# Performance work log

Hardware: AMD Instinct MI355X
Metric: run time of the kernel (lower is better)

The kernel has to match this reference:

```python
import jax, jax.numpy as jnp
import numpy as np

HEAD_SIZE = 64
D_MODEL = 768


def setup_inputs() -> dict:
    key = jax.random.key(0)
    ks = jax.random.split(key, 7)
    x = jax.random.normal(ks[0], (8, 4096, D_MODEL), dtype=jnp.float32)
    def lin_init(kw, kb, fan_in, fan_out):
        bound = 1.0 / np.sqrt(fan_in)
        W = jax.random.uniform(kw, (fan_in, fan_out), minval=-bound, maxval=bound, dtype=jnp.float32)
        b = jax.random.uniform(kb, (fan_out,), minval=-bound, maxval=bound, dtype=jnp.float32)
        return W, b
    Wq, bq = lin_init(ks[1], ks[2], D_MODEL, HEAD_SIZE)
    Wk, bk = lin_init(ks[3], ks[4], D_MODEL, HEAD_SIZE)
    Wv, bv = lin_init(ks[5], ks[6], D_MODEL, HEAD_SIZE)
    return {"x": x, "Wq": Wq, "bq": bq, "Wk": Wk, "bk": bk, "Wv": Wv, "bv": bv}


def reference(x, Wq, bq, Wk, bk, Wv, bv):
    # x: [B, N, 768]; projections to [B, N, head_size]
    q = jnp.einsum("bnd,dh->bnh", x, Wq) + bq
    k = jnp.einsum("bnd,dh->bnh", x, Wk) + bk
    v = jnp.einsum("bnd,dh->bnh", x, Wv) + bv
    scale = 1.0 / jnp.sqrt(jnp.asarray(q.shape[-1], dtype=q.dtype))
    wei = jnp.einsum("bqh,bkh->bqk", q, k) * scale  # [B, N, N]
    wei = jax.nn.softmax(wei, axis=-1)
    out = jnp.einsum("bqk,bkh->bqh", wei, v)  # [B, N, head_size]
    return out
```

## Files before the change

### kernel.cpp

```cpp
#include <hip/hip_runtime.h>
#include <stdint.h>
#include <stddef.h>

typedef __bf16 bf16x8 __attribute__((ext_vector_type(8)));
typedef __bf16 bf16x4 __attribute__((ext_vector_type(4)));
typedef float  f32x4  __attribute__((ext_vector_type(4)));

#define MFMA16(A, B, C) __builtin_amdgcn_mfma_f32_16x16x32_bf16((A), (B), (C), 0, 0, 0)

#define QSCALE 0.18033688011112042f

#if __has_builtin(__builtin_amdgcn_exp2f)
__device__ __forceinline__ float fast_exp2(float x) {
    return __builtin_amdgcn_exp2f(x);
}
#else
__device__ __forceinline__ float fast_exp2(float x) {
    float r;
    asm("v_exp_f32 %0, %1" : "=v"(r) : "v"(x));
    return r;
}
#endif

__device__ __forceinline__ void async_copy16(__bf16* lds, const __bf16* g) {
    __builtin_amdgcn_global_load_lds(
        (const __attribute__((address_space(1))) void*)g,
        (__attribute__((address_space(3))) void*)lds,
        16, 0, 0);
}

__global__ __launch_bounds__(256) void qkv_proj_kernel(
    const float* __restrict__ x,
    const float* __restrict__ Wq, const float* __restrict__ bq,
    const float* __restrict__ Wk, const float* __restrict__ bk,
    const float* __restrict__ Wv, const float* __restrict__ bv,
    __bf16* __restrict__ Qg, __bf16* __restrict__ Kg, __bf16* __restrict__ Vcg)
{
    __shared__ __bf16 xs[64][40];
    __shared__ __bf16 wt[192][40];

    const int tid  = threadIdx.x;
    const int wid  = tid >> 6;
    const int lane = tid & 63;
    const int l15  = lane & 15;
    const int l4   = lane >> 4;
    const int m0   = blockIdx.x * 64;

    f32x4 acc[4][3];
    #pragma unroll
    for (int i = 0; i < 4; ++i)
        #pragma unroll
        for (int j = 0; j < 3; ++j)
            acc[i][j] = (f32x4){0.f, 0.f, 0.f, 0.f};

    for (int k0 = 0; k0 < 768; k0 += 32) {
        #pragma unroll
        for (int i = 0; i < 2; ++i) {
            int idx = tid + 256 * i;
            int row = idx >> 3;
            int c4  = idx & 7;
            const float4 v = *reinterpret_cast<const float4*>(
                x + (size_t)(m0 + row) * 768 + k0 + c4 * 4);
            bf16x4 t;
            t[0] = (__bf16)v.x; t[1] = (__bf16)v.y;
            t[2] = (__bf16)v.z; t[3] = (__bf16)v.w;
            *reinterpret_cast<bf16x4*>(&xs[row][c4 * 4]) = t;
        }
        #pragma unroll
        for (int i = 0; i < 6; ++i) {
            int idx = tid + 256 * i;
            int kg  = idx / 192;
            int c   = idx - kg * 192;
            const float* Wm = (c < 64) ? Wq : ((c < 128) ? Wk : Wv);
            int cc = c & 63;
            bf16x4 t;
            #pragma unroll
            for (int j = 0; j < 4; ++j)
                t[j] = (__bf16)Wm[(size_t)(k0 + kg * 4 + j) * 64 + cc];
            *reinterpret_cast<bf16x4*>(&wt[c][kg * 4]) = t;
        }
        __syncthreads();

        bf16x8 afrag[4];
        #pragma unroll
        for (int rf = 0; rf < 4; ++rf)
            afrag[rf] = *reinterpret_cast<const bf16x8*>(&xs[rf * 16 + l15][l4 * 8]);
        #pragma unroll
        for (int cf = 0; cf < 3; ++cf) {
            bf16x8 bfrag = *reinterpret_cast<const bf16x8*>(
                &wt[wid * 48 + cf * 16 + l15][l4 * 8]);
            #pragma unroll
            for (int rf = 0; rf < 4; ++rf)
                acc[rf][cf] = MFMA16(afrag[rf], bfrag, acc[rf][cf]);
        }
        __syncthreads();
    }

    #pragma unroll
    for (int cf = 0; cf < 3; ++cf) {
        int col = wid * 48 + cf * 16 + l15;
        int mi  = col >> 6;
        int h   = col & 63;
        float bias = (mi == 0) ? bq[h] : ((mi == 1) ? bk[h] : bv[h]);
        float scl  = (mi == 0) ? QSCALE : 1.0f;
        #pragma unroll
        for (int rf = 0; rf < 4; ++rf) {
            int r0 = rf * 16 + l4 * 4;
            if (mi == 2) {
                int m  = m0 + r0;
                int bb = m >> 12;
                int n0 = m & 4095;
                int c  = n0 >> 5;
                int goff = ((l4 ^ (h & 3)) * 8) + (rf & 1) * 4;
                bf16x4 t;
                #pragma unroll
                for (int r = 0; r < 4; ++r)
                    t[r] = (__bf16)(acc[rf][cf][r] + bias);
                *reinterpret_cast<bf16x4*>(
                    Vcg + (((size_t)bb * 128 + c) * 64 + h) * 32 + goff) = t;
            } else {
                __bf16* G = (mi == 0) ? Qg : Kg;
                #pragma unroll
                for (int r = 0; r < 4; ++r)
                    G[(size_t)(m0 + r0 + r) * 64 + h] =
                        (__bf16)((acc[rf][cf][r] + bias) * scl);
            }
        }
    }
}

__global__ __launch_bounds__(256, 2) void attn_kernel(
    const __bf16* __restrict__ Qg, const __bf16* __restrict__ Kg,
    const __bf16* __restrict__ Vcg, float* __restrict__ out)
{
    __shared__ __align__(16) char smem[65536];
    __bf16* ksbase = reinterpret_cast<__bf16*>(smem);
    __bf16* vsbase = ksbase + 4 * 2 * 32 * 64;

    const int tid  = threadIdx.x;
    const int wid  = tid >> 6;
    const int lane = tid & 63;
    const int l15  = lane & 15;
    const int l4   = lane >> 4;
    const int ks   = wid;
    const int b    = blockIdx.x & 7;
    const int qt   = blockIdx.x >> 3;
    const int q0   = qt * 64;

    const __bf16* Kb = Kg  + (size_t)b * 4096 * 64;
    const __bf16* Vb = Vcg + (size_t)b * 128 * 2048;

    __bf16* kst0 = ksbase + (ks * 2 + 0) * 32 * 64;
    __bf16* kst1 = ksbase + (ks * 2 + 1) * 32 * 64;
    __bf16* vst0 = vsbase + (ks * 2 + 0) * 64 * 32;
    __bf16* vst1 = vsbase + (ks * 2 + 1) * 64 * 32;

    int koff[2][2], voff[4];
    #pragma unroll
    for (int dc = 0; dc < 2; ++dc)
        #pragma unroll
        for (int cf = 0; cf < 2; ++cf) {
            int row = cf * 16 + l15;
            koff[dc][cf] = row * 64 + (((dc * 4 + l4) ^ (row & 7)) * 8);
        }
    #pragma unroll
    for (int ht = 0; ht < 4; ++ht) {
        int row = ht * 16 + l15;
        voff[ht] = row * 32 + ((l4 ^ (row & 3)) * 8);
    }

    const int krow = lane >> 3;
    const int kg_s = (lane & 7) ^ (lane >> 3);
    const int vlin = lane * 16;

    auto issue_K = [&](__bf16* kp, int c) {
        #pragma unroll
        for (int j = 0; j < 4; ++j)
            async_copy16(kp + j * 8 * 64,
                         Kb + (size_t)(c * 32 + j * 8 + krow) * 64 + kg_s * 8);
    };
    auto issue_V = [&](__bf16* vp, int c) {
        const __bf16* src = Vb + (size_t)c * 2048;
        #pragma unroll
        for (int j = 0; j < 4; ++j)
            async_copy16(vp + j * 512, src + j * 512 + (lane & 63) * 8);
    };

    bf16x8 aq[4][2];
    #pragma unroll
    for (int set = 0; set < 4; ++set)
        #pragma unroll
        for (int dc = 0; dc < 2; ++dc)
            aq[set][dc] = *reinterpret_cast<const bf16x8*>(
                Qg + (size_t)(b * 4096 + q0 + set * 16 + l15) * 64 + dc * 32 + l4 * 8);

    f32x4 lacc[4];
    f32x4 o[4][4];
    #pragma unroll
    for (int set = 0; set < 4; ++set) {
        lacc[set] = (f32x4){0.f, 0.f, 0.f, 0.f};
        #pragma unroll
        for (int ht = 0; ht < 4; ++ht)
            o[set][ht] = (f32x4){0.f, 0.f, 0.f, 0.f};
    }

    const int c0 = ks * 32;
    issue_K(kst0, c0);
    issue_V(vst0, c0);

    for (int t = 0; t < 32; ++t) {
        const __bf16* kp = (t & 1) ? kst1 : kst0;
        const __bf16* vp = (t & 1) ? vst1 : vst0;
        __bf16* kpn = (t & 1) ? kst0 : kst1;
        __bf16* vpn = (t & 1) ? vst0 : vst1;
        const bool pre = (t + 1) < 32;

        asm volatile("s_waitcnt vmcnt(4)" ::: "memory");
        __builtin_amdgcn_sched_barrier(0);

        bf16x8 kfr[2][2];
        #pragma unroll
        for (int dc = 0; dc < 2; ++dc)
            #pragma unroll
            for (int cf = 0; cf < 2; ++cf)
                kfr[dc][cf] = *reinterpret_cast<const bf16x8*>(kp + koff[dc][cf]);

        if (pre) issue_K(kpn, c0 + t + 1);

        f32x4 s[4][2];
        #pragma unroll
        for (int set = 0; set < 4; ++set)
            #pragma unroll
            for (int cf = 0; cf < 2; ++cf)
                s[set][cf] = (f32x4){0.f, 0.f, 0.f, 0.f};
        __builtin_amdgcn_s_setprio(1);
        #pragma unroll
        for (int dc = 0; dc < 2; ++dc)
            #pragma unroll
            for (int cf = 0; cf < 2; ++cf)
                #pragma unroll
                for (int set = 0; set < 4; ++set)
                    s[set][cf] = MFMA16(kfr[dc][cf], aq[set][dc], s[set][cf]);
        __builtin_amdgcn_s_setprio(0);

        #pragma unroll
        for (int set = 0; set < 4; ++set) {
            #pragma unroll
            for (int cf = 0; cf < 2; ++cf)
                #pragma unroll
                for (int r = 0; r < 4; ++r)
                    s[set][cf][r] = fast_exp2(s[set][cf][r]);
            lacc[set] += s[set][0];
            lacc[set] += s[set][1];
        }

        bf16x8 pb[4];
        #pragma unroll
        for (int set = 0; set < 4; ++set)
            #pragma unroll
            for (int j = 0; j < 4; ++j) {
                pb[set][j]     = (__bf16)s[set][0][j];
                pb[set][j + 4] = (__bf16)s[set][1][j];
            }

        if (pre) {
            asm volatile("s_waitcnt vmcnt(4)" ::: "memory");
        } else {
            asm volatile("s_waitcnt vmcnt(0)" ::: "memory");
        }
        __builtin_amdgcn_sched_barrier(0);

        bf16x8 vfr[4];
        #pragma unroll
        for (int ht = 0; ht < 4; ++ht)
            vfr[ht] = *reinterpret_cast<const bf16x8*>(vp + voff[ht]);

        if (pre) issue_V(vpn, c0 + t + 1);

        __builtin_amdgcn_s_setprio(1);
        #pragma unroll
        for (int ht = 0; ht < 4; ++ht)
            #pragma unroll
            for (int set = 0; set < 4; ++set)
                o[set][ht] = MFMA16(vfr[ht], pb[set], o[set][ht]);
        __builtin_amdgcn_s_setprio(0);
    }

    float lw[4];
    #pragma unroll
    for (int set = 0; set < 4; ++set) {
        float v = lacc[set][0] + lacc[set][1] + lacc[set][2] + lacc[set][3];
        v += __shfl_xor(v, 16);
        v += __shfl_xor(v, 32);
        lw[set] = v;
    }

    __syncthreads();
    float* lbuf = reinterpret_cast<float*>(smem);
    float* obuf = lbuf + 256;
    const int hcol = 4 * l4;

    if (l4 == 0) {
        #pragma unroll
        for (int set = 0; set < 4; ++set)
            lbuf[ks * 64 + set * 16 + l15] = lw[set];
    }
    #pragma unroll
    for (int k = 1; k < 4; ++k) {
        if (ks == k) {
            #pragma unroll
            for (int set = 0; set < 4; ++set)
                #pragma unroll
                for (int ht = 0; ht < 4; ++ht)
                    *reinterpret_cast<f32x4*>(
                        &obuf[(set * 16 + l15) * 68 + ht * 16 + hcol]) = o[set][ht];
        }
        __syncthreads();
        if (ks == 0) {
            #pragma unroll
            for (int set = 0; set < 4; ++set)
                #pragma unroll
                for (int ht = 0; ht < 4; ++ht) {
                    f32x4 p = *reinterpret_cast<const f32x4*>(
                        &obuf[(set * 16 + l15) * 68 + ht * 16 + hcol]);
                    o[set][ht][0] += p[0]; o[set][ht][1] += p[1];
                    o[set][ht][2] += p[2]; o[set][ht][3] += p[3];
                }
        }
        __syncthreads();
    }

    if (ks == 0) {
        #pragma unroll
        for (int set = 0; set < 4; ++set) {
            int q = set * 16 + l15;
            float L = lbuf[q] + lbuf[64 + q] + lbuf[128 + q] + lbuf[192 + q];
            float inv = 1.0f / L;
            #pragma unroll
            for (int ht = 0; ht < 4; ++ht) {
                f32x4 acc = o[set][ht];
                acc[0] *= inv; acc[1] *= inv; acc[2] *= inv; acc[3] *= inv;
                *reinterpret_cast<f32x4*>(
                    out + (size_t)(b * 4096 + q0 + q) * 64 + ht * 16 + hcol) = acc;
            }
        }
    }
}

extern "C" void kernel_launch(void* const* d_in, const int* in_sizes, int n_in,
                              void* d_out, int out_size, void* d_ws, size_t ws_size,
                              hipStream_t stream)
{
    (void)in_sizes; (void)n_in; (void)out_size; (void)ws_size;
    const float* x  = (const float*)d_in[0];
    const float* Wq = (const float*)d_in[1];
    const float* bq = (const float*)d_in[2];
    const float* Wk = (const float*)d_in[3];
    const float* bk = (const float*)d_in[4];
    const float* Wv = (const float*)d_in[5];
    const float* bv = (const float*)d_in[6];
    float* out = (float*)d_out;

    __bf16* Qg  = (__bf16*)d_ws;
    __bf16* Kg  = Qg + (size_t)32768 * 64;
    __bf16* Vcg = Kg + (size_t)32768 * 64;

    qkv_proj_kernel<<<512, 256, 0, stream>>>(x, Wq, bq, Wk, bk, Wv, bv, Qg, Kg, Vcg);
    attn_kernel<<<512, 256, 0, stream>>>(Qg, Kg, Vcg, out);
}
```

Baseline: 71.26 us.

## Triple-buffer K tiles in LDS to prefetch two chunks ahead

K staging goes from double to triple buffering, so the K tile for step t+2 is fetched while step t computes. V stays double-buffered, and the buffers now rotate through pointer swaps instead of parity selects. The vmcnt waits are rewritten to match the deeper pipeline, and a scheduling barrier is added after the Q loads. The aim is to hide more global-load latency, at the cost of raising LDS per block to 80KB, which only just fits two blocks per CU.

Result: no change. 72.13 us (+1.2%).

```diff
diff --git a/kernel.cpp b/kernel.cpp
--- a/kernel.cpp
+++ b/kernel.cpp
@@ -133,9 +133,9 @@
     const __bf16* __restrict__ Qg, const __bf16* __restrict__ Kg,
     const __bf16* __restrict__ Vcg, float* __restrict__ out)
 {
-    __shared__ __align__(16) char smem[65536];
+    __shared__ __align__(16) char smem[81920];
     __bf16* ksbase = reinterpret_cast<__bf16*>(smem);
-    __bf16* vsbase = ksbase + 4 * 2 * 32 * 64;
+    __bf16* vsbase = ksbase + 4 * 3 * 32 * 64;
 
     const int tid  = threadIdx.x;
     const int wid  = tid >> 6;
@@ -150,8 +150,9 @@
     const __bf16* Kb = Kg  + (size_t)b * 4096 * 64;
     const __bf16* Vb = Vcg + (size_t)b * 128 * 2048;
 
-    __bf16* kst0 = ksbase + (ks * 2 + 0) * 32 * 64;
-    __bf16* kst1 = ksbase + (ks * 2 + 1) * 32 * 64;
+    __bf16* kstA = ksbase + (ks * 3 + 0) * 32 * 64;
+    __bf16* kstB = ksbase + (ks * 3 + 1) * 32 * 64;
+    __bf16* kstC = ksbase + (ks * 3 + 2) * 32 * 64;
     __bf16* vst0 = vsbase + (ks * 2 + 0) * 64 * 32;
     __bf16* vst1 = vsbase + (ks * 2 + 1) * 64 * 32;
 
@@ -171,7 +172,6 @@
 
     const int krow = lane >> 3;
     const int kg_s = (lane & 7) ^ (lane >> 3);
-    const int vlin = lane * 16;
 
     auto issue_K = [&](__bf16* kp, int c) {
         #pragma unroll
@@ -193,6 +193,7 @@
         for (int dc = 0; dc < 2; ++dc)
             aq[set][dc] = *reinterpret_cast<const bf16x8*>(
                 Qg + (size_t)(b * 4096 + q0 + set * 16 + l15) * 64 + dc * 32 + l4 * 8);
+    __builtin_amdgcn_sched_barrier(0);
 
     f32x4 lacc[4];
     f32x4 o[4][4];
@@ -205,17 +206,18 @@
     }
 
     const int c0 = ks * 32;
-    issue_K(kst0, c0);
+    issue_K(kstA, c0);
     issue_V(vst0, c0);
+    issue_K(kstB, c0 + 1);
+
+    __bf16 *kcur = kstA, *knx1 = kstB, *knx2 = kstC;
+    __bf16 *vcur = vst0, *vnxt = vst1;
 
     for (int t = 0; t < 32; ++t) {
-        const __bf16* kp = (t & 1) ? kst1 : kst0;
-        const __bf16* vp = (t & 1) ? vst1 : vst0;
-        __bf16* kpn = (t & 1) ? kst0 : kst1;
-        __bf16* vpn = (t & 1) ? vst0 : vst1;
-        const bool pre = (t + 1) < 32;
-
-        asm volatile("s_waitcnt vmcnt(4)" ::: "memory");
+        const bool preK = (t + 2) < 32;
+        const bool preV = (t + 1) < 32;
+
+        asm volatile("s_waitcnt vmcnt(8)" ::: "memory");
         __builtin_amdgcn_sched_barrier(0);
 
         bf16x8 kfr[2][2];
@@ -223,9 +225,9 @@
         for (int dc = 0; dc < 2; ++dc)
             #pragma unroll
             for (int cf = 0; cf < 2; ++cf)
-                kfr[dc][cf] = *reinterpret_cast<const bf16x8*>(kp + koff[dc][cf]);
-
-        if (pre) issue_K(kpn, c0 + t + 1);
+                kfr[dc][cf] = *reinterpret_cast<const bf16x8*>(kcur + koff[dc][cf]);
+
+        if (preK) issue_K(knx2, c0 + t + 2);
 
         f32x4 s[4][2];
         #pragma unroll
@@ -263,7 +265,7 @@
                 pb[set][j + 4] = (__bf16)s[set][1][j];
             }
 
-        if (pre) {
+        if (t < 30) {
             asm volatile("s_waitcnt vmcnt(4)" ::: "memory");
         } else {
             asm volatile("s_waitcnt vmcnt(0)" ::: "memory");
@@ -273,9 +275,9 @@
         bf16x8 vfr[4];
         #pragma unroll
         for (int ht = 0; ht < 4; ++ht)
-            vfr[ht] = *reinterpret_cast<const bf16x8*>(vp + voff[ht]);
-
-        if (pre) issue_V(vpn, c0 + t + 1);
+            vfr[ht] = *reinterpret_cast<const bf16x8*>(vcur + voff[ht]);
+
+        if (preV) issue_V(vnxt, c0 + t + 1);
 
         __builtin_amdgcn_s_setprio(1);
         #pragma unroll
@@ -284,6 +286,9 @@
             for (int set = 0; set < 4; ++set)
                 o[set][ht] = MFMA16(vfr[ht], pb[set], o[set][ht]);
         __builtin_amdgcn_s_setprio(0);
+
+        __bf16* tmp = kcur; kcur = knx1; knx1 = knx2; knx2 = tmp;
+        __bf16* tv = vcur; vcur = vnxt; vnxt = tv;
     }
 
     float lw[4];
```
